# Kernel optimization log

Hardware: AMD Instinct MI355X
Metric: run time of the kernel (lower is better)

The kernel has to match this reference:

```python
import jax, jax.numpy as jnp
import numpy as np

LN_EPS = 1e-5
BN_EPS = 1e-5


def setup_inputs() -> dict:
    key = jax.random.key(0)
    k0, k1, k2, k3 = jax.random.split(key, 4)
    N, C, T, V, S = 128, 64, 128, 25, 3  # batch, channels, frames, joints, subsets
    rel = C // 8                          # rel_channels = 8
    inner = rel * S                       # hidden_dim * n_heads = 24
    x = jax.random.normal(k0, (N, C, T, V), dtype=jnp.float32)
    # graph adjacency parameter (3 subsets over 25 joints); small positive values
    PA = jax.random.uniform(k1, (S, V, V), dtype=jnp.float32) * 0.1
    ln_gamma = jnp.ones((C,), jnp.float32)
    ln_beta = jnp.zeros((C,), jnp.float32)
    # to_qk: Linear(C, 2*inner), weight init normal(0, 1) per source
    Wqk = jax.random.normal(k2, (2 * inner, C), dtype=jnp.float32)
    bqk = jnp.zeros((2 * inner,), jnp.float32)
    # conv_branch_init: normal(0, sqrt(2/(out*1*1*branches)))
    conv_w = jax.random.normal(k3, (S, C, C), dtype=jnp.float32) * np.float32(np.sqrt(2.0 / (C * S)))
    conv_b = jnp.zeros((S, C), jnp.float32)
    bn_gamma = jnp.ones((C,), jnp.float32)
    bn_beta = jnp.zeros((C,), jnp.float32)
    bn_mean = jnp.zeros((C,), jnp.float32)
    bn_var = jnp.ones((C,), jnp.float32)
    return {"x": x, "PA": PA, "ln_gamma": ln_gamma, "ln_beta": ln_beta,
            "Wqk": Wqk, "bqk": bqk, "conv_w": conv_w, "conv_b": conv_b,
            "bn_gamma": bn_gamma, "bn_beta": bn_beta, "bn_mean": bn_mean, "bn_var": bn_var}


def reference(x, PA, ln_gamma, ln_beta, Wqk, bqk, conv_w, conv_b,
              bn_gamma, bn_beta, bn_mean, bn_var):
    N, C, T, V = x.shape
    S = PA.shape[0]                       # num_subset == n_heads
    rel = Wqk.shape[0] // (2 * S)         # hidden dim per head
    scale = rel ** (-0.5)

    xv = jnp.transpose(x, (0, 2, 3, 1))   # n t v c

    # --- SelfAttention: LayerNorm -> Linear -> per-head softmax(q k^T) ---
    mu = jnp.mean(xv, axis=-1, keepdims=True)
    var = jnp.mean(jnp.square(xv - mu), axis=-1, keepdims=True)
    yn = (xv - mu) * jax.lax.rsqrt(var + LN_EPS) * ln_gamma + ln_beta
    qk = yn @ Wqk.T + bqk                 # n t v (2*inner)
    inner = qk.shape[-1] // 2
    q = qk[..., :inner].reshape(N, T, V, S, rel)
    k = qk[..., inner:].reshape(N, T, V, S, rel)
    dots = jnp.einsum('ntihd,ntjhd->nthij', q, k) * scale  # (n,t,h,V,V)
    attn = jax.nn.softmax(dots, axis=-1)

    # --- attention-modulated adjacency + per-subset aggregation ---
    A = attn * PA[None, None]             # (n,t,h,V,V)
    z = jnp.einsum('nthij,ntjc->nthic', A, xv)  # (n,t,h,V,C) messages per subset
    # per-subset 1x1 conv then sum over subsets
    out = jnp.einsum('nthvc,hoc->notv', z, conv_w) \
        + jnp.sum(conv_b, axis=0)[None, :, None, None]  # (n,C,t,V)

    # --- BatchNorm2d (eval-mode with provided stats) + residual + ReLU ---
    bn_out = (out - bn_mean[None, :, None, None]) \
        * jax.lax.rsqrt(bn_var + BN_EPS)[None, :, None, None] \
        * bn_gamma[None, :, None, None] + bn_beta[None, :, None, None]
    return jax.nn.relu(bn_out + x)        # down is identity since in_c == out_c
```

## Files before the change

kernel.cpp:

```cpp
#include <hip/hip_runtime.h>
#include <hip/hip_bf16.h>
#include <math.h>

typedef __attribute__((ext_vector_type(8))) short bf16x8;
typedef __attribute__((ext_vector_type(4))) float f32x4;

__device__ inline unsigned short f2bf(float f) {
    return __builtin_bit_cast(unsigned short, __float2bfloat16(f));
}
__device__ inline float bf2f(unsigned short u) {
    return __bfloat162float(__builtin_bit_cast(__hip_bfloat16, u));
}
__device__ inline bf16x8 cvt8(float4 a, float4 b) {
    bf16x8 r;
    r[0]=(short)f2bf(a.x); r[1]=(short)f2bf(a.y); r[2]=(short)f2bf(a.z); r[3]=(short)f2bf(a.w);
    r[4]=(short)f2bf(b.x); r[5]=(short)f2bf(b.y); r[6]=(short)f2bf(b.z); r[7]=(short)f2bf(b.w);
    return r;
}
__device__ inline void split8(float4 a, float4 b, bf16x8& hi, bf16x8& lo) {
    float f[8] = {a.x,a.y,a.z,a.w,b.x,b.y,b.z,b.w};
    #pragma unroll
    for (int i = 0; i < 8; ++i) {
        unsigned short h = f2bf(f[i]);
        hi[i] = (short)h;
        lo[i] = (short)f2bf(f[i] - bf2f(h));
    }
}

#define LDS_FLOATS 7755

__global__ __launch_bounds__(256, 5)
void agcn_fused_kernel(const float* __restrict__ x,
                       const float* __restrict__ PA,
                       const float* __restrict__ ln_g, const float* __restrict__ ln_b,
                       const float* __restrict__ Wqk, const float* __restrict__ bqk,
                       const float* __restrict__ conv_w, const float* __restrict__ conv_b,
                       const float* __restrict__ bn_g, const float* __restrict__ bn_b,
                       const float* __restrict__ bn_m, const float* __restrict__ bn_v,
                       float* __restrict__ out)
{
    __shared__ float lds[LDS_FLOATS];
    float* xv = lds;
    unsigned short* ynh  = (unsigned short*)(lds + 1700);
    unsigned short* ynl  = (unsigned short*)(lds + 2500);
    float* qkb  = lds + 3300;
    unsigned short* xvT  = (unsigned short*)(lds + 4600);
    float* Abuf = lds + 5880;
    unsigned short* A_bf = (unsigned short*)(lds + 1700);
    unsigned short* zA   = (unsigned short*)(lds + 1700);
    float* res  = lds + 5880;

    const int bid = blockIdx.x;
    const int n = bid >> 7, t = bid & 127;
    const int tid = threadIdx.x;
    const int lane = tid & 63, w = tid >> 6;
    const int g = lane >> 4, l15 = lane & 15;
    const int o = 16 * w + l15;

    float4 cw_f[12];
    #pragma unroll
    for (int kt = 0; kt < 6; ++kt) {
        const float* wp = &conv_w[(kt >> 1) * 4096 + o * 64 + (kt & 1) * 32 + 8 * g];
        cw_f[2*kt]   = *(const float4*)wp;
        cw_f[2*kt+1] = *(const float4*)(wp + 4);
    }
    float4 wq_f[4];
    float bq = 0.f;
    if (w < 3) {
        const int j = 16 * w + l15;
        #pragma unroll
        for (int ks = 0; ks < 2; ++ks) {
            const float* wp = &Wqk[j * 64 + ks * 32 + 8 * g];
            wq_f[2*ks]   = *(const float4*)wp;
            wq_f[2*ks+1] = *(const float4*)(wp + 4);
        }
        bq = bqk[j];
    }
    const int c0 = (lane & 7) << 3;
    const float4 lg0 = *(const float4*)&ln_g[c0];
    const float4 lg1 = *(const float4*)&ln_g[c0 + 4];
    const float4 lb0 = *(const float4*)&ln_b[c0];
    const float4 lb1 = *(const float4*)&ln_b[c0 + 4];
    const float sc_e = bn_g[o] * rsqrtf(bn_v[o] + 1e-5f);
    const float bi_e = (conv_b[o] + conv_b[64 + o] + conv_b[128 + o]) * sc_e
                       + bn_b[o] - bn_m[o] * sc_e;

    {
        const float* xb = x + (size_t)n * 204800 + t * 25;
        for (int idx = tid; idx < 1600; idx += 256) {
            int c = idx / 25, v = idx - c * 25;
            xv[v * 68 + c] = xb[c * 3200 + v];
        }
    }

    bf16x8 cw[6];
    #pragma unroll
    for (int kt = 0; kt < 6; ++kt) cw[kt] = cvt8(cw_f[2*kt], cw_f[2*kt+1]);
    bf16x8 wqh[2], wql[2];
    if (w < 3) {
        #pragma unroll
        for (int ks = 0; ks < 2; ++ks) split8(wq_f[2*ks], wq_f[2*ks+1], wqh[ks], wql[ks]);
    }
    __syncthreads();

    {
        const int v = (w << 3) + (lane >> 3);
        if (v < 25) {
            const float4* xp = (const float4*)&xv[v * 68 + c0];
            float4 a = xp[0], b = xp[1];
            float s1 = ((a.x + a.y) + (a.z + a.w)) + ((b.x + b.y) + (b.z + b.w));
            float s2 = ((a.x*a.x + a.y*a.y) + (a.z*a.z + a.w*a.w))
                     + ((b.x*b.x + b.y*b.y) + (b.z*b.z + b.w*b.w));
            s1 += __shfl_xor(s1, 1);  s2 += __shfl_xor(s2, 1);
            s1 += __shfl_xor(s1, 2);  s2 += __shfl_xor(s2, 2);
            s1 += __shfl_xor(s1, 4);  s2 += __shfl_xor(s2, 4);
            float mu = s1 * (1.0f / 64.0f);
            float var = s2 * (1.0f / 64.0f) - mu * mu;
            float rstd = rsqrtf(var + 1e-5f);
            float xa[8] = {a.x,a.y,a.z,a.w,b.x,b.y,b.z,b.w};
            float lg[8] = {lg0.x,lg0.y,lg0.z,lg0.w,lg1.x,lg1.y,lg1.z,lg1.w};
            float lb[8] = {lb0.x,lb0.y,lb0.z,lb0.w,lb1.x,lb1.y,lb1.z,lb1.w};
            bf16x8 hh8, ll8;
            #pragma unroll
            for (int i = 0; i < 8; ++i) {
                float y = (xa[i] - mu) * rstd * lg[i] + lb[i];
                unsigned short hh = f2bf(y);
                hh8[i] = (short)hh;
                ll8[i] = (short)f2bf(y - bf2f(hh));
            }
            int base = (v * 64 + c0) ^ ((v & 7) << 3);
            *(bf16x8*)&ynh[base] = hh8;
            *(bf16x8*)&ynl[base] = ll8;
        }
        int c = tid >> 2, j0 = (tid & 3) << 3;
        bf16x8 pk;
        #pragma unroll
        for (int i = 0; i < 8; ++i) {
            int j = j0 + i;
            pk[i] = (j < 25) ? (short)f2bf(xv[j * 68 + c]) : (short)0;
        }
        *(bf16x8*)&xvT[c * 40 + j0] = pk;
    }
    __syncthreads();

    if (w < 3) {
        const int j = 16 * w + l15;
        #pragma unroll
        for (int mt = 0; mt < 2; ++mt) {
            f32x4 acc = {bq, bq, bq, bq};
            #pragma unroll
            for (int ks = 0; ks < 2; ++ks) {
                int row = 16 * mt + l15;
                int idx = (row * 64 + ks * 32 + 8 * g) ^ ((row & 7) << 3);
                bf16x8 ah = *(bf16x8*)&ynh[idx];
                bf16x8 al = *(bf16x8*)&ynl[idx];
                acc = __builtin_amdgcn_mfma_f32_16x16x32_bf16(al, wqh[ks], acc, 0, 0, 0);
                acc = __builtin_amdgcn_mfma_f32_16x16x32_bf16(ah, wql[ks], acc, 0, 0, 0);
                acc = __builtin_amdgcn_mfma_f32_16x16x32_bf16(ah, wqh[ks], acc, 0, 0, 0);
            }
            #pragma unroll
            for (int reg = 0; reg < 4; ++reg) {
                int v = 16 * mt + 4 * g + reg;
                if (v < 25) qkb[v * 52 + j] = acc[reg];
            }
        }
    }
    __syncthreads();

    for (int idx = tid; idx < 1875; idx += 256) {
        int h = idx / 625, r = idx - h * 625;
        int i = r / 25, j = r - i * 25;
        const float4* q = (const float4*)&qkb[i * 52 + h * 8];
        const float4* kp = (const float4*)&qkb[j * 52 + 24 + h * 8];
        float4 q0 = q[0], q1 = q[1], k0 = kp[0], k1 = kp[1];
        float d = q0.x*k0.x + q0.y*k0.y + q0.z*k0.z + q0.w*k0.w
                + q1.x*k1.x + q1.y*k1.y + q1.z*k1.z + q1.w*k1.w;
        Abuf[idx] = d * 0.35355339059327373f;
    }
    __syncthreads();

    if (tid < 150) {
        int r = tid >> 1, hf = tid & 1;
        int h = (r < 25) ? 0 : ((r < 50) ? 1 : 2);
        int i = r - h * 25;
        int j0 = hf ? 13 : 0;
        const float* row = &Abuf[r * 25];
        const float* pa = &PA[h * 625 + i * 25];
        float rr[13];
        #pragma unroll
        for (int j = 0; j < 13; ++j) {
            int jj = j0 + j;
            rr[j] = (jj < 25) ? row[jj] : -3.0e38f;
        }
        float m0 = fmaxf(rr[0], rr[1]), m1 = fmaxf(rr[2], rr[3]);
        float m2 = fmaxf(rr[4], rr[5]), m3 = fmaxf(rr[6], rr[7]);
        float m4 = fmaxf(rr[8], rr[9]), m5 = fmaxf(rr[10], rr[11]);
        float m = fmaxf(fmaxf(fmaxf(m0, m1), fmaxf(m2, m3)),
                        fmaxf(fmaxf(m4, m5), rr[12]));
        m = fmaxf(m, __shfl_xor(m, 1));
        float e[13];
        float s0 = 0.f, s1 = 0.f;
        #pragma unroll
        for (int j = 0; j < 12; j += 2) {
            e[j]   = __expf(rr[j]   - m); s0 += e[j];
            e[j+1] = __expf(rr[j+1] - m); s1 += e[j+1];
        }
        e[12] = __expf(rr[12] - m);
        float s = (s0 + s1) + e[12];
        s += __shfl_xor(s, 1);
        float inv = 1.0f / s;
        unsigned short* ar = &A_bf[r * 40];
        #pragma unroll
        for (int j = 0; j < 13; ++j) {
            int jj = j0 + j;
            if (jj < 25) ar[jj] = f2bf(e[j] * inv * pa[jj]);
        }
        if (hf) {
            #pragma unroll
            for (int j = 25; j < 32; ++j) ar[j] = 0;
        }
    }
    __syncthreads();

    f32x4 zacc[5];
    {
        bf16x8 bfrag = *(bf16x8*)&xvT[(16 * w + l15) * 40 + 8 * g];
        #pragma unroll
        for (int mt = 0; mt < 5; ++mt) {
            bf16x8 afrag = *(bf16x8*)&A_bf[(16 * mt + l15) * 40 + 8 * g];
            f32x4 a = {0.f, 0.f, 0.f, 0.f};
            zacc[mt] = __builtin_amdgcn_mfma_f32_16x16x32_bf16(afrag, bfrag, a, 0, 0, 0);
        }
    }
    __syncthreads();

    #pragma unroll
    for (int mt = 0; mt < 5; ++mt) {
        #pragma unroll
        for (int reg = 0; reg < 4; ++reg) {
            int r = 16 * mt + 4 * g + reg;
            if (r < 75) {
                int h = (r < 25) ? 0 : ((r < 50) ? 1 : 2);
                int i = r - h * 25;
                zA[i * 200 + h * 64 + 16 * w + l15] = f2bf(zacc[mt][reg]);
            }
        }
    }
    __syncthreads();

    {
        const int r1 = (16 + l15 < 25) ? (16 + l15) : 0;
        f32x4 acc0 = {0.f, 0.f, 0.f, 0.f}, acc1 = {0.f, 0.f, 0.f, 0.f};
        #pragma unroll
        for (int kt = 0; kt < 6; ++kt) {
            bf16x8 a0 = *(bf16x8*)&zA[l15 * 200 + 32 * kt + 8 * g];
            bf16x8 a1 = *(bf16x8*)&zA[r1 * 200 + 32 * kt + 8 * g];
            acc0 = __builtin_amdgcn_mfma_f32_16x16x32_bf16(a0, cw[kt], acc0, 0, 0, 0);
            acc1 = __builtin_amdgcn_mfma_f32_16x16x32_bf16(a1, cw[kt], acc1, 0, 0, 0);
        }
        #pragma unroll
        for (int reg = 0; reg < 4; ++reg) {
            int v = 4 * g + reg;
            float val = acc0[reg] * sc_e + bi_e + xv[v * 68 + o];
            res[o * 25 + v] = fmaxf(val, 0.f);
        }
        #pragma unroll
        for (int reg = 0; reg < 4; ++reg) {
            int v = 16 + 4 * g + reg;
            if (v < 25) {
                float val = acc1[reg] * sc_e + bi_e + xv[v * 68 + o];
                res[o * 25 + v] = fmaxf(val, 0.f);
            }
        }
    }
    __syncthreads();

    {
        float* ob = out + (size_t)n * 204800 + t * 25;
        for (int idx = tid; idx < 1600; idx += 256) {
            int c = idx / 25, v = idx - c * 25;
            ob[c * 3200 + v] = res[idx];
        }
    }
}

extern "C" void kernel_launch(void* const* d_in, const int* in_sizes, int n_in,
                              void* d_out, int out_size, void* d_ws, size_t ws_size,
                              hipStream_t stream) {
    const float* x      = (const float*)d_in[0];
    const float* PA     = (const float*)d_in[1];
    const float* ln_g   = (const float*)d_in[2];
    const float* ln_b   = (const float*)d_in[3];
    const float* Wqk    = (const float*)d_in[4];
    const float* bqk    = (const float*)d_in[5];
    const float* conv_w = (const float*)d_in[6];
    const float* conv_b = (const float*)d_in[7];
    const float* bn_g   = (const float*)d_in[8];
    const float* bn_b   = (const float*)d_in[9];
    const float* bn_m   = (const float*)d_in[10];
    const float* bn_v   = (const float*)d_in[11];
    float* outp = (float*)d_out;

    agcn_fused_kernel<<<dim3(128 * 128), dim3(256), 0, stream>>>(
        x, PA, ln_g, ln_b, Wqk, bqk, conv_w, conv_b,
        bn_g, bn_b, bn_m, bn_v, outp);
}
```

Before: 270.8 us.

## Shrink LDS footprint, fuse dot-products into softmax, write output directly

Cuts the shared-memory allocation by removing the transposed bf16 copy of x, the score buffer and the output staging buffer, and raises launch bounds to 8 waves per SIMD so more blocks can be resident. Attention scores are now computed inside the softmax threads, which removes one barrier and an LDS round trip. The MFMA B fragment is built straight from xv, and results are stored to global memory directly from the MFMA accumulators instead of through LDS. The costs are redundant q/k loads per row, less coalesced strided global stores, and possible register pressure or spills under the tighter launch bound.

```diff
diff --git a/kernel.cpp b/kernel.cpp
--- a/kernel.cpp
+++ b/kernel.cpp
@@ -27,9 +27,9 @@
     }
 }
 
-#define LDS_FLOATS 7755
-
-__global__ __launch_bounds__(256, 5)
+#define LDS_FLOATS 4528
+
+__global__ __launch_bounds__(256, 8)
 void agcn_fused_kernel(const float* __restrict__ x,
                        const float* __restrict__ PA,
                        const float* __restrict__ ln_g, const float* __restrict__ ln_b,
@@ -41,14 +41,11 @@
 {
     __shared__ float lds[LDS_FLOATS];
     float* xv = lds;
-    unsigned short* ynh  = (unsigned short*)(lds + 1700);
-    unsigned short* ynl  = (unsigned short*)(lds + 2500);
-    float* qkb  = lds + 3300;
-    unsigned short* xvT  = (unsigned short*)(lds + 4600);
-    float* Abuf = lds + 5880;
-    unsigned short* A_bf = (unsigned short*)(lds + 1700);
-    unsigned short* zA   = (unsigned short*)(lds + 1700);
-    float* res  = lds + 5880;
+    unsigned short* ynh  = (unsigned short*)(lds + 1628);
+    unsigned short* ynl  = (unsigned short*)(lds + 2428);
+    unsigned short* A_bf = (unsigned short*)(lds + 1628);
+    unsigned short* zA   = (unsigned short*)(lds + 1628);
+    float* qkb = lds + 3228;
 
     const int bid = blockIdx.x;
     const int n = bid >> 7, t = bid & 127;
@@ -89,7 +86,7 @@
         const float* xb = x + (size_t)n * 204800 + t * 25;
         for (int idx = tid; idx < 1600; idx += 256) {
             int c = idx / 25, v = idx - c * 25;
-            xv[v * 68 + c] = xb[c * 3200 + v];
+            xv[v * 65 + c] = xb[c * 3200 + v];
         }
     }
 
@@ -104,20 +101,20 @@
     __syncthreads();
 
     {
-        const int v = (w << 3) + (lane >> 3);
-        if (v < 25) {
-            const float4* xp = (const float4*)&xv[v * 68 + c0];
-            float4 a = xp[0], b = xp[1];
-            float s1 = ((a.x + a.y) + (a.z + a.w)) + ((b.x + b.y) + (b.z + b.w));
-            float s2 = ((a.x*a.x + a.y*a.y) + (a.z*a.z + a.w*a.w))
-                     + ((b.x*b.x + b.y*b.y) + (b.z*b.z + b.w*b.w));
+        const int vr = (w << 3) + (lane >> 3);
+        if (vr < 25) {
+            float xa[8];
+            #pragma unroll
+            for (int i = 0; i < 8; ++i) xa[i] = xv[vr * 65 + c0 + i];
+            float s1 = ((xa[0]+xa[1])+(xa[2]+xa[3])) + ((xa[4]+xa[5])+(xa[6]+xa[7]));
+            float s2 = ((xa[0]*xa[0]+xa[1]*xa[1])+(xa[2]*xa[2]+xa[3]*xa[3]))
+                     + ((xa[4]*xa[4]+xa[5]*xa[5])+(xa[6]*xa[6]+xa[7]*xa[7]));
             s1 += __shfl_xor(s1, 1);  s2 += __shfl_xor(s2, 1);
             s1 += __shfl_xor(s1, 2);  s2 += __shfl_xor(s2, 2);
             s1 += __shfl_xor(s1, 4);  s2 += __shfl_xor(s2, 4);
             float mu = s1 * (1.0f / 64.0f);
             float var = s2 * (1.0f / 64.0f) - mu * mu;
             float rstd = rsqrtf(var + 1e-5f);
-            float xa[8] = {a.x,a.y,a.z,a.w,b.x,b.y,b.z,b.w};
             float lg[8] = {lg0.x,lg0.y,lg0.z,lg0.w,lg1.x,lg1.y,lg1.z,lg1.w};
             float lb[8] = {lb0.x,lb0.y,lb0.z,lb0.w,lb1.x,lb1.y,lb1.z,lb1.w};
             bf16x8 hh8, ll8;
@@ -128,18 +125,10 @@
                 hh8[i] = (short)hh;
                 ll8[i] = (short)f2bf(y - bf2f(hh));
             }
-            int base = (v * 64 + c0) ^ ((v & 7) << 3);
+            int base = (vr * 64 + c0) ^ ((vr & 7) << 3);
             *(bf16x8*)&ynh[base] = hh8;
             *(bf16x8*)&ynl[base] = ll8;
         }
-        int c = tid >> 2, j0 = (tid & 3) << 3;
-        bf16x8 pk;
-        #pragma unroll
-        for (int i = 0; i < 8; ++i) {
-            int j = j0 + i;
-            pk[i] = (j < 25) ? (short)f2bf(xv[j * 68 + c]) : (short)0;
-        }
-        *(bf16x8*)&xvT[c * 40 + j0] = pk;
     }
     __syncthreads();
 
@@ -167,53 +156,45 @@
     }
     __syncthreads();
 
-    for (int idx = tid; idx < 1875; idx += 256) {
-        int h = idx / 625, r = idx - h * 625;
-        int i = r / 25, j = r - i * 25;
-        const float4* q = (const float4*)&qkb[i * 52 + h * 8];
-        const float4* kp = (const float4*)&qkb[j * 52 + 24 + h * 8];
-        float4 q0 = q[0], q1 = q[1], k0 = kp[0], k1 = kp[1];
-        float d = q0.x*k0.x + q0.y*k0.y + q0.z*k0.z + q0.w*k0.w
-                + q1.x*k1.x + q1.y*k1.y + q1.z*k1.z + q1.w*k1.w;
-        Abuf[idx] = d * 0.35355339059327373f;
-    }
-    __syncthreads();
-
     if (tid < 150) {
         int r = tid >> 1, hf = tid & 1;
         int h = (r < 25) ? 0 : ((r < 50) ? 1 : 2);
         int i = r - h * 25;
-        int j0 = hf ? 13 : 0;
-        const float* row = &Abuf[r * 25];
+        const float4* qp = (const float4*)&qkb[i * 52 + h * 8];
+        float4 q0 = qp[0], q1 = qp[1];
+        const int j0 = hf ? 13 : 0;
+        const int cnt = hf ? 12 : 13;
         const float* pa = &PA[h * 625 + i * 25];
         float rr[13];
         #pragma unroll
-        for (int j = 0; j < 13; ++j) {
-            int jj = j0 + j;
-            rr[j] = (jj < 25) ? row[jj] : -3.0e38f;
-        }
-        float m0 = fmaxf(rr[0], rr[1]), m1 = fmaxf(rr[2], rr[3]);
-        float m2 = fmaxf(rr[4], rr[5]), m3 = fmaxf(rr[6], rr[7]);
-        float m4 = fmaxf(rr[8], rr[9]), m5 = fmaxf(rr[10], rr[11]);
+        for (int jj = 0; jj < 13; ++jj) {
+            int j = j0 + jj;
+            int jc = (j < 25) ? j : 0;
+            const float4* kp = (const float4*)&qkb[jc * 52 + 24 + h * 8];
+            float4 k0 = kp[0], k1 = kp[1];
+            float d = q0.x*k0.x + q0.y*k0.y + q0.z*k0.z + q0.w*k0.w
+                    + q1.x*k1.x + q1.y*k1.y + q1.z*k1.z + q1.w*k1.w;
+            rr[jj] = (jj < cnt) ? d * 0.35355339059327373f : -3.0e38f;
+        }
+        float m0 = fmaxf(rr[0], rr[1]),  m1 = fmaxf(rr[2], rr[3]);
+        float m2 = fmaxf(rr[4], rr[5]),  m3 = fmaxf(rr[6], rr[7]);
+        float m4 = fmaxf(rr[8], rr[9]),  m5 = fmaxf(rr[10], rr[11]);
         float m = fmaxf(fmaxf(fmaxf(m0, m1), fmaxf(m2, m3)),
                         fmaxf(fmaxf(m4, m5), rr[12]));
         m = fmaxf(m, __shfl_xor(m, 1));
-        float e[13];
-        float s0 = 0.f, s1 = 0.f;
-        #pragma unroll
-        for (int j = 0; j < 12; j += 2) {
-            e[j]   = __expf(rr[j]   - m); s0 += e[j];
-            e[j+1] = __expf(rr[j+1] - m); s1 += e[j+1];
-        }
-        e[12] = __expf(rr[12] - m);
-        float s = (s0 + s1) + e[12];
+        float s = 0.f;
+        #pragma unroll
+        for (int jj = 0; jj < 13; ++jj) {
+            rr[jj] = __expf(rr[jj] - m);
+            s += rr[jj];
+        }
         s += __shfl_xor(s, 1);
         float inv = 1.0f / s;
         unsigned short* ar = &A_bf[r * 40];
         #pragma unroll
-        for (int j = 0; j < 13; ++j) {
-            int jj = j0 + j;
-            if (jj < 25) ar[jj] = f2bf(e[j] * inv * pa[jj]);
+        for (int jj = 0; jj < 13; ++jj) {
+            int j = j0 + jj;
+            if (jj < cnt) ar[j] = f2bf(rr[jj] * inv * pa[j]);
         }
         if (hf) {
             #pragma unroll
@@ -224,7 +205,12 @@
 
     f32x4 zacc[5];
     {
-        bf16x8 bfrag = *(bf16x8*)&xvT[(16 * w + l15) * 40 + 8 * g];
+        bf16x8 bfrag;
+        #pragma unroll
+        for (int i = 0; i < 8; ++i) {
+            int j = 8 * g + i;
+            bfrag[i] = (j < 25) ? (short)f2bf(xv[j * 65 + o]) : (short)0;
+        }
         #pragma unroll
         for (int mt = 0; mt < 5; ++mt) {
             bf16x8 afrag = *(bf16x8*)&A_bf[(16 * mt + l15) * 40 + 8 * g];
@@ -258,28 +244,20 @@
             acc0 = __builtin_amdgcn_mfma_f32_16x16x32_bf16(a0, cw[kt], acc0, 0, 0, 0);
             acc1 = __builtin_amdgcn_mfma_f32_16x16x32_bf16(a1, cw[kt], acc1, 0, 0, 0);
         }
+        float* ob = out + (size_t)n * 204800 + (size_t)o * 3200 + t * 25;
         #pragma unroll
         for (int reg = 0; reg < 4; ++reg) {
             int v = 4 * g + reg;
-            float val = acc0[reg] * sc_e + bi_e + xv[v * 68 + o];
-            res[o * 25 + v] = fmaxf(val, 0.f);
+            float val = acc0[reg] * sc_e + bi_e + xv[v * 65 + o];
+            ob[v] = fmaxf(val, 0.f);
         }
         #pragma unroll
         for (int reg = 0; reg < 4; ++reg) {
             int v = 16 + 4 * g + reg;
             if (v < 25) {
-                float val = acc1[reg] * sc_e + bi_e + xv[v * 68 + o];
-                res[o * 25 + v] = fmaxf(val, 0.f);
-            }
-        }
-    }
-    __syncthreads();
-
-    {
-        float* ob = out + (size_t)n * 204800 + t * 25;
-        for (int idx = tid; idx < 1600; idx += 256) {
-            int c = idx / 25, v = idx - c * 25;
-            ob[c * 3200 + v] = res[idx];
+                float val = acc1[reg] * sc_e + bi_e + xv[v * 65 + o];
+                ob[v] = fmaxf(val, 0.f);
+            }
         }
     }
 }
```

After: 497.7 us. 83.8% more time.
